# Kernel tuning notes

Hardware: AMD Instinct MI355X
Metric: run time of the kernel (lower is better)

Reference implementation:

```python
import jax, jax.numpy as jnp
import numpy as np

D, M, K, L, H, BS = 128, 8, 256, 2, 256, 1024


def setup_inputs() -> dict:
    key = jax.random.key(0)
    ks = jax.random.split(key, 7)
    s_d = 1.0 / np.sqrt(D)
    s_2d = 1.0 / np.sqrt(2 * D)
    s_h = 1.0 / np.sqrt(H)
    x = jax.random.normal(ks[0], (BS, D), jnp.float32)
    codebook0 = jax.random.uniform(ks[1], (K, D), jnp.float32, -s_d, s_d)
    codebooks = jax.random.uniform(ks[2], (M - 1, K, D), jnp.float32, -s_d, s_d)
    Wc = jax.random.uniform(ks[3], (M - 1, D, 2 * D), jnp.float32, -s_2d, s_2d)
    bc = jax.random.uniform(ks[4], (M - 1, D), jnp.float32, -s_2d, s_2d)
    W1 = jax.random.uniform(ks[5], (M - 1, L, H, D), jnp.float32, -s_d, s_d)
    W2 = jax.random.uniform(ks[6], (M - 1, L, D, H), jnp.float32, -s_h, s_h)
    return {"x": x, "codebook0": codebook0, "codebooks": codebooks,
            "Wc": Wc, "bc": bc, "W1": W1, "W2": W2}


def _step_targets(xhat, cb, Wc_m, bc_m, W1_m, W2_m):
    """Candidate quantization targets for one step. xhat:[bs,d], cb:[K,d] -> [bs,K,d].
    MLPconcat(concat(zqs, xhat)) is split into the zqs part and the xhat part so the
    [bs*K, 2d] repeat of the torch code is never materialized (same math)."""
    Wz, Wx = Wc_m[:, :D], Wc_m[:, D:]          # Linear(2d,d): y = cc @ W.T + b
    z = cb[None, :, :] + (cb @ Wz.T)[None, :, :] + (xhat @ Wx.T)[:, None, :] + bc_m  # [bs,K,d]
    for l in range(L):
        z = z + jnp.maximum(jnp.einsum('bkd,hd->bkh', z, W1_m[l]), 0.0) @ W2_m[l].T
    return z + xhat[:, None, :]


def _encode(x, codebook0, codebooks, Wc, bc, W1, W2):
    # step 0: plain nearest-centroid assignment (assign_to_codebook)
    d0 = (x * x).sum(-1, keepdims=True) + (codebook0 * codebook0).sum(-1) - 2.0 * x @ codebook0.T
    code0 = jnp.argmin(d0, axis=1)
    xhat = codebook0[code0]
    codes = [code0]
    xn = (x * x).sum(-1, keepdims=True)        # [bs,1]
    for m in range(M - 1):
        z = _step_targets(xhat, codebooks[m], Wc[m], bc[m], W1[m], W2[m])  # [bs,K,d]
        dist = xn + (z * z).sum(-1) - 2.0 * jnp.einsum('bd,bkd->bk', x, z)
        idx = jnp.argmin(dist, axis=1)
        xhat = jnp.take_along_axis(z, idx[:, None, None], axis=1)[:, 0, :]
        codes.append(idx)
    return jnp.stack(codes, axis=1)            # [bs, M] int


def _decode(codes, codebook0, codebooks, Wc, bc, W1, W2):
    xhat = codebook0[codes[:, 0]]
    side = [xhat]
    for m in range(M - 1):
        zq = codebooks[m][codes[:, m + 1]]     # [bs,d]
        Wz, Wx = Wc[m][:, :D], Wc[m][:, D:]
        z = zq + zq @ Wz.T + xhat @ Wx.T + bc[m]
        for l in range(L):
            z = z + jnp.maximum(z @ W1[m, l].T, 0.0) @ W2[m, l].T
        xhat = xhat + z
        side.append(xhat)
    return xhat, side


def reference(x, codebook0, codebooks, Wc, bc, W1, W2):
    # forward(): encode under no_grad, then differentiable decode with side outputs
    codes = jax.lax.stop_gradient(_encode(x, codebook0, codebooks, Wc, bc, W1, W2))
    xhat, side = _decode(codes, codebook0, codebooks, Wc, bc, W1, W2)
    return (xhat, codes, tuple(side))
```

## Files before the change

### kernel.cpp

```cpp
#include <hip/hip_runtime.h>


typedef _Float16 f16;
typedef f16 half4_t __attribute__((ext_vector_type(4)));
typedef f16 half8_t __attribute__((ext_vector_type(8)));
typedef float f32x16 __attribute__((ext_vector_type(16)));

#define OUT_CODES 131072
#define OUT_SIDE  139264

#define WS_XHAT  0
#define WS_RB    131072
#define WS_Y     262144
#define WS_ZC    393216
#define WS_BESTD 425984
#define WS_BESTI 430080
#define WS_BESTZ 434176
#define WS_WSPLIT 960000
#define NW1 458752

#define HLO 8192

__device__ __forceinline__ f32x16 mfma_f16(half8_t a, half8_t b, f32x16 c) {
  return __builtin_amdgcn_mfma_f32_32x32x16_f16(a, b, c, 0, 0, 0);
}

__global__ __launch_bounds__(256) void k_wsplit(const float* __restrict__ W1,
    const float* __restrict__ W2, f16* __restrict__ wsh)
{
  int i = (blockIdx.x * 256 + threadIdx.x) * 4;
  const float* src;
  f16* hi;
  if (i < NW1) { src = W1 + i; hi = wsh + i; }
  else         { src = W2 + (i - NW1); hi = wsh + 2 * NW1 + (i - NW1); }
  f16* lo = hi + NW1;
  float4 v = *(const float4*)src;
  half4_t h, l;
  float s;
  s = v.x * 256.f; h[0] = (f16)s; l[0] = (f16)(s - (float)h[0]);
  s = v.y * 256.f; h[1] = (f16)s; l[1] = (f16)(s - (float)h[1]);
  s = v.z * 256.f; h[2] = (f16)s; l[2] = (f16)(s - (float)h[2]);
  s = v.w * 256.f; h[3] = (f16)s; l[3] = (f16)(s - (float)h[3]);
  *(half4_t*)hi = h;
  *(half4_t*)lo = l;
}

__global__ __launch_bounds__(256) void k_step0(const float* __restrict__ x,
    const float* __restrict__ cb0, float* __restrict__ ws, float* __restrict__ out)
{
  __shared__ float xs[128];
  __shared__ float redv[4];
  __shared__ int   redi[4];
  __shared__ int   kwin;
  int tx = threadIdx.x, b = blockIdx.x;
  if (tx < 128) xs[tx] = x[b * 128 + tx];
  __syncthreads();
  const float* c = cb0 + tx * 128;
  float s = 0.f;
  for (int d = 0; d < 128; d += 4) {
    float4 cv = *(const float4*)(c + d);
    float4 xv = *(const float4*)(xs + d);
    float a0 = xv.x - cv.x, a1 = xv.y - cv.y, a2 = xv.z - cv.z, a3 = xv.w - cv.w;
    s += a0 * a0 + a1 * a1 + a2 * a2 + a3 * a3;
  }
  float v = s; int idx = tx;
  for (int off = 32; off; off >>= 1) {
    float v2 = __shfl_xor(v, off);
    int   i2 = __shfl_xor(idx, off);
    if (v2 < v || (v2 == v && i2 < idx)) { v = v2; idx = i2; }
  }
  if ((tx & 63) == 0) { redv[tx >> 6] = v; redi[tx >> 6] = idx; }
  __syncthreads();
  if (tx == 0) {
    float bv = redv[0]; int bi = redi[0];
    for (int w = 1; w < 4; w++)
      if (redv[w] < bv || (redv[w] == bv && redi[w] < bi)) { bv = redv[w]; bi = redi[w]; }
    kwin = bi;
    out[OUT_CODES + b * 8] = (float)bi;
  }
  __syncthreads();
  int k = kwin;
  if (tx < 128) {
    float xh = cb0[k * 128 + tx];
    ws[WS_XHAT + b * 128 + tx] = xh;
    ws[WS_RB   + b * 128 + tx] = xs[tx] - xh;
    out[OUT_SIDE + b * 128 + tx] = xh;
  }
}

__global__ __launch_bounds__(128) void k_prep(const float* __restrict__ cb,
    const float* __restrict__ Wc, const float* __restrict__ bcm, float* __restrict__ ws)
{
  __shared__ float row[128];
  int tx = threadIdx.x, blk = blockIdx.x;
  if (blk < 256) {
    row[tx] = cb[blk * 128 + tx];
    __syncthreads();
    const float* wrow = Wc + tx * 256;
    float s = 0.f;
    for (int d = 0; d < 128; d += 4) {
      float4 wv = *(const float4*)(wrow + d);
      float4 zv = *(const float4*)(row + d);
      s += wv.x * zv.x + wv.y * zv.y + wv.z * zv.z + wv.w * zv.w;
    }
    ws[WS_ZC + blk * 128 + tx] = row[tx] + s + bcm[tx];
  } else {
    int b = blk - 256;
    row[tx] = ws[WS_XHAT + b * 128 + tx];
    __syncthreads();
    const float* wrow = Wc + tx * 256 + 128;
    float s = 0.f;
    for (int d = 0; d < 128; d += 4) {
      float4 wv = *(const float4*)(wrow + d);
      float4 zv = *(const float4*)(row + d);
      s += wv.x * zv.x + wv.y * zv.y + wv.z * zv.z + wv.w * zv.w;
    }
    ws[WS_Y + b * 128 + tx] = s;
  }
}

__global__ __launch_bounds__(256, 2) void k_step(const f16* __restrict__ wsh,
    float* __restrict__ ws, int sm)
{
  __shared__ __align__(16) f16 lds[32768];
  f16* Zh = lds;
  f16* Zl = lds + HLO;
  f16* Hh = lds + 2 * HLO;
  f16* Hl = lds + 3 * HLO;
  int tx = threadIdx.x;
  int lane = tx & 63, w = tx >> 6;
  int col = lane & 31, koct = lane >> 5;
  int b = blockIdx.x >> 2, t = blockIdx.x & 3, k0 = t << 6;

  {
    const float* zc = ws + WS_ZC + k0 * 128;
    const float* y  = ws + WS_Y + b * 128;
    for (int idx = tx; idx < 1024; idx += 256) {
      int m = idx & 63, d0 = (idx >> 6) << 3;
      float4 a  = *(const float4*)(zc + m * 128 + d0);
      float4 bb = *(const float4*)(zc + m * 128 + d0 + 4);
      float4 ya = *(const float4*)(y + d0);
      float4 yb = *(const float4*)(y + d0 + 4);
      float sv[8] = {a.x + ya.x, a.y + ya.y, a.z + ya.z, a.w + ya.w,
                     bb.x + yb.x, bb.y + yb.y, bb.z + yb.z, bb.w + yb.w};
      half8_t h8, l8;
#pragma unroll
      for (int j = 0; j < 8; j++) {
        float v = sv[j] * 256.f;
        f16 h = (f16)v; h8[j] = h; l8[j] = (f16)(v - (float)h);
      }
      int c0 = (d0 + ((m & 15) << 3)) & 127;
      *(half8_t*)(Zh + (m << 7) + c0) = h8;
      *(half8_t*)(Zl + (m << 7) + c0) = l8;
    }
  }
  __syncthreads();

  const int rot0 = (col & 15) << 3;
  const f16* Zr0 = Zh + (col << 7);
  const f16* Zr1 = Zh + ((col + 32) << 7);
  const f16* Hr0 = Hh + (col << 7);
  const f16* Hr1 = Hh + ((col + 32) << 7);

  for (int l = 0; l < 2; l++) {
    const f16* w1h = wsh + (size_t)((sm * 2 + l) * 256) * 128;
    const f16* w2h = wsh + 2 * NW1 + (size_t)((sm * 2 + l) * 128) * 256;
    f32x16 acc2[2];
#pragma unroll
    for (int i = 0; i < 16; i++) { acc2[0][i] = 0.f; acc2[1][i] = 0.f; }

#pragma unroll
    for (int hf = 0; hf < 2; hf++) {
      const f16* a1p = w1h + (size_t)((hf << 7) + (w << 5) + col) * 128 + (koct << 3);
      const f16* a2p = w2h + (size_t)((w << 5) + col) * 256 + (hf << 7) + (koct << 3);
      half8_t a1hv[8], a1lv[8], a2hv[8], a2lv[8];
#pragma unroll
      for (int kc = 0; kc < 8; kc++) {
        a1hv[kc] = *(const half8_t*)(a1p + (kc << 4));
        a1lv[kc] = *(const half8_t*)(a1p + NW1 + (kc << 4));
      }
#pragma unroll
      for (int kc = 0; kc < 8; kc++) {
        a2hv[kc] = *(const half8_t*)(a2p + (kc << 4));
        a2lv[kc] = *(const half8_t*)(a2p + NW1 + (kc << 4));
      }

      f32x16 acc1[2];
#pragma unroll
      for (int i = 0; i < 16; i++) { acc1[0][i] = 0.f; acc1[1][i] = 0.f; }
#pragma unroll
      for (int kc = 0; kc < 8; kc++) {
        int poff = (((kc << 4) + (koct << 3)) + rot0) & 127;
        half8_t bh0 = *(const half8_t*)(Zr0 + poff);
        half8_t bl0 = *(const half8_t*)(Zr0 + HLO + poff);
        half8_t bh1 = *(const half8_t*)(Zr1 + poff);
        half8_t bl1 = *(const half8_t*)(Zr1 + HLO + poff);
        acc1[0] = mfma_f16(a1hv[kc], bh0, acc1[0]);
        acc1[1] = mfma_f16(a1hv[kc], bh1, acc1[1]);
        acc1[0] = mfma_f16(a1lv[kc], bh0, acc1[0]);
        acc1[1] = mfma_f16(a1lv[kc], bh1, acc1[1]);
        acc1[0] = mfma_f16(a1hv[kc], bl0, acc1[0]);
        acc1[1] = mfma_f16(a1hv[kc], bl1, acc1[1]);
      }
#pragma unroll
      for (int mt = 0; mt < 2; mt++) {
        int m = (mt << 5) + col;
#pragma unroll
        for (int qd = 0; qd < 4; qd++) {
          half4_t hv, lv;
#pragma unroll
          for (int j = 0; j < 4; j++) {
            float tv = fmaxf(acc1[mt][(qd << 2) + j], 0.f) * 0.00390625f;
            f16 h = (f16)tv; hv[j] = h; lv[j] = (f16)(tv - (float)h);
          }
          int c = (((w << 5) + (qd << 3) + (koct << 2)) + rot0) & 127;
          *(half4_t*)(Hh + (m << 7) + c) = hv;
          *(half4_t*)(Hl + (m << 7) + c) = lv;
        }
      }
      __syncthreads();
#pragma unroll
      for (int kc = 0; kc < 8; kc++) {
        int poff = (((kc << 4) + (koct << 3)) + rot0) & 127;
        half8_t bh0 = *(const half8_t*)(Hr0 + poff);
        half8_t bl0 = *(const half8_t*)(Hr0 + HLO + poff);
        half8_t bh1 = *(const half8_t*)(Hr1 + poff);
        half8_t bl1 = *(const half8_t*)(Hr1 + HLO + poff);
        acc2[0] = mfma_f16(a2hv[kc], bh0, acc2[0]);
        acc2[1] = mfma_f16(a2hv[kc], bh1, acc2[1]);
        acc2[0] = mfma_f16(a2lv[kc], bh0, acc2[0]);
        acc2[1] = mfma_f16(a2lv[kc], bh1, acc2[1]);
        acc2[0] = mfma_f16(a2hv[kc], bl0, acc2[0]);
        acc2[1] = mfma_f16(a2hv[kc], bl1, acc2[1]);
      }
      __syncthreads();
    }
#pragma unroll
    for (int mt = 0; mt < 2; mt++) {
      int m = (mt << 5) + col;
      f16* zhr = Zh + (m << 7);
      f16* zlr = Zl + (m << 7);
#pragma unroll
      for (int qd = 0; qd < 4; qd++) {
        int c = (((w << 5) + (qd << 3) + (koct << 2)) + rot0) & 127;
        half4_t zh = *(half4_t*)(zhr + c);
        half4_t zl = *(half4_t*)(zlr + c);
#pragma unroll
        for (int j = 0; j < 4; j++) {
          float zs = (float)zh[j] + (float)zl[j];
          zs += acc2[mt][(qd << 2) + j] * 0.00390625f;
          f16 h = (f16)zs; zh[j] = h; zl[j] = (f16)(zs - (float)h);
        }
        *(half4_t*)(zhr + c) = zh;
        *(half4_t*)(zlr + c) = zl;
      }
    }
    __syncthreads();
  }

  float* pd = (float*)Hh;
  int* rwin = (int*)Hh + 64;
  {
    int row = tx >> 2, seg = tx & 3;
    int rotr = (row & 15) << 3;
    const f16* zhr = Zh + (row << 7);
    const f16* zlr = Zl + (row << 7);
    const float* rb = ws + WS_RB + b * 128 + (seg << 5);
    float s = 0.f;
#pragma unroll
    for (int o = 0; o < 4; o++) {
      int c = (((seg << 5) + (o << 3)) + rotr) & 127;
      half8_t zh = *(const half8_t*)(zhr + c);
      half8_t zl = *(const half8_t*)(zlr + c);
      float4 r0 = *(const float4*)(rb + (o << 3));
      float4 r1 = *(const float4*)(rb + (o << 3) + 4);
      float rr[8] = {r0.x, r0.y, r0.z, r0.w, r1.x, r1.y, r1.z, r1.w};
#pragma unroll
      for (int j = 0; j < 8; j++) {
        float z = ((float)zh[j] + (float)zl[j]) * 0.00390625f;
        float dlt = rr[j] - z;
        s += dlt * dlt;
      }
    }
    s += __shfl_xor(s, 1);
    s += __shfl_xor(s, 2);
    if (seg == 0) pd[row] = s;
  }
  __syncthreads();
  if (tx < 64) {
    float v = pd[tx]; int idx = tx;
#pragma unroll
    for (int off = 32; off; off >>= 1) {
      float v2 = __shfl_xor(v, off);
      int   i2 = __shfl_xor(idx, off);
      if (v2 < v || (v2 == v && i2 < idx)) { v = v2; idx = i2; }
    }
    if (tx == 0) {
      ws[WS_BESTD + (b << 2) + t] = v;
      ((int*)ws)[WS_BESTI + (b << 2) + t] = k0 + idx;
      rwin[0] = idx;
    }
  }
  __syncthreads();
  if (tx < 32) {
    int rw = rwin[0];
    int c = ((tx << 2) + ((rw & 15) << 3)) & 127;
    half4_t zh = *(const half4_t*)(Zh + (rw << 7) + c);
    half4_t zl = *(const half4_t*)(Zl + (rw << 7) + c);
    float4 z;
    z.x = ((float)zh[0] + (float)zl[0]) * 0.00390625f;
    z.y = ((float)zh[1] + (float)zl[1]) * 0.00390625f;
    z.z = ((float)zh[2] + (float)zl[2]) * 0.00390625f;
    z.w = ((float)zh[3] + (float)zl[3]) * 0.00390625f;
    *(float4*)(ws + WS_BESTZ + (((b << 2) + t) << 7) + (tx << 2)) = z;
  }
}

__global__ __launch_bounds__(128) void k_update(const float* __restrict__ x,
    float* __restrict__ ws, float* __restrict__ out, int m, int last)
{
  __shared__ int tsel;
  int tx = threadIdx.x, b = blockIdx.x;
  if (tx == 0) {
    float bv = ws[WS_BESTD + (b << 2)]; int bt = 0;
    for (int q = 1; q < 4; q++) {
      float v = ws[WS_BESTD + (b << 2) + q];
      if (v < bv) { bv = v; bt = q; }
    }
    tsel = bt;
    int k = ((const int*)ws)[WS_BESTI + (b << 2) + bt];
    out[OUT_CODES + b * 8 + (m + 1)] = (float)k;
  }
  __syncthreads();
  int bt = tsel;
  float z  = ws[WS_BESTZ + (((b << 2) + bt) << 7) + tx];
  float xh = ws[WS_XHAT + b * 128 + tx] + z;
  ws[WS_XHAT + b * 128 + tx] = xh;
  ws[WS_RB   + b * 128 + tx] = x[b * 128 + tx] - xh;
  out[OUT_SIDE + (m + 1) * 131072 + b * 128 + tx] = xh;
  if (last) out[b * 128 + tx] = xh;
}

extern "C" void kernel_launch(void* const* d_in, const int* in_sizes, int n_in,
                              void* d_out, int out_size, void* d_ws, size_t ws_size,
                              hipStream_t stream)
{
  const float* x   = (const float*)d_in[0];
  const float* cb0 = (const float*)d_in[1];
  const float* cbs = (const float*)d_in[2];
  const float* Wc  = (const float*)d_in[3];
  const float* bc  = (const float*)d_in[4];
  const float* W1  = (const float*)d_in[5];
  const float* W2  = (const float*)d_in[6];
  float* out = (float*)d_out;
  float* ws  = (float*)d_ws;
  f16* wsh = (f16*)(ws + WS_WSPLIT);

  k_wsplit<<<896, 256, 0, stream>>>(W1, W2, wsh);
  k_step0<<<1024, 256, 0, stream>>>(x, cb0, ws, out);
  for (int m = 0; m < 7; m++) {
    k_prep<<<1280, 128, 0, stream>>>(cbs + m * 256 * 128, Wc + m * 128 * 256,
                                     bc + m * 128, ws);
    k_step<<<4096, 256, 0, stream>>>(wsh, ws, m);
    k_update<<<1024, 128, 0, stream>>>(x, ws, out, m, (m == 6) ? 1 : 0);
  }
}
```

Before: 2.151 ms.

## Software-pipeline MLP hidden halves and raise wave priority around MFMA loops

```diff
diff --git a/kernel.cpp b/kernel.cpp
--- a/kernel.cpp
+++ b/kernel.cpp
@@ -169,72 +169,147 @@
 #pragma unroll
     for (int i = 0; i < 16; i++) { acc2[0][i] = 0.f; acc2[1][i] = 0.f; }
 
-#pragma unroll
-    for (int hf = 0; hf < 2; hf++) {
-      const f16* a1p = w1h + (size_t)((hf << 7) + (w << 5) + col) * 128 + (koct << 3);
-      const f16* a2p = w2h + (size_t)((w << 5) + col) * 256 + (hf << 7) + (koct << 3);
-      half8_t a1hv[8], a1lv[8], a2hv[8], a2lv[8];
+    half8_t a1hv[8], a1lv[8];
+    {
+      const f16* a1p = w1h + (size_t)((w << 5) + col) * 128 + (koct << 3);
 #pragma unroll
       for (int kc = 0; kc < 8; kc++) {
         a1hv[kc] = *(const half8_t*)(a1p + (kc << 4));
         a1lv[kc] = *(const half8_t*)(a1p + NW1 + (kc << 4));
       }
+    }
+
+    f32x16 acc1[2];
+#pragma unroll
+    for (int i = 0; i < 16; i++) { acc1[0][i] = 0.f; acc1[1][i] = 0.f; }
+    __builtin_amdgcn_s_setprio(1);
+#pragma unroll
+    for (int kc = 0; kc < 8; kc++) {
+      int poff = (((kc << 4) + (koct << 3)) + rot0) & 127;
+      half8_t bh0 = *(const half8_t*)(Zr0 + poff);
+      half8_t bl0 = *(const half8_t*)(Zr0 + HLO + poff);
+      half8_t bh1 = *(const half8_t*)(Zr1 + poff);
+      half8_t bl1 = *(const half8_t*)(Zr1 + HLO + poff);
+      acc1[0] = mfma_f16(a1hv[kc], bh0, acc1[0]);
+      acc1[1] = mfma_f16(a1hv[kc], bh1, acc1[1]);
+      acc1[0] = mfma_f16(a1lv[kc], bh0, acc1[0]);
+      acc1[1] = mfma_f16(a1lv[kc], bh1, acc1[1]);
+      acc1[0] = mfma_f16(a1hv[kc], bl0, acc1[0]);
+      acc1[1] = mfma_f16(a1hv[kc], bl1, acc1[1]);
+    }
+    __builtin_amdgcn_s_setprio(0);
+
+    half8_t a2hv[8], a2lv[8];
+    {
+      const f16* a2p = w2h + (size_t)((w << 5) + col) * 256 + (koct << 3);
 #pragma unroll
       for (int kc = 0; kc < 8; kc++) {
         a2hv[kc] = *(const half8_t*)(a2p + (kc << 4));
         a2lv[kc] = *(const half8_t*)(a2p + NW1 + (kc << 4));
       }
-
-      f32x16 acc1[2];
-#pragma unroll
-      for (int i = 0; i < 16; i++) { acc1[0][i] = 0.f; acc1[1][i] = 0.f; }
+    }
+    half8_t b1hv[8], b1lv[8];
+    {
+      const f16* b1p = w1h + (size_t)(128 + (w << 5) + col) * 128 + (koct << 3);
 #pragma unroll
       for (int kc = 0; kc < 8; kc++) {
-        int poff = (((kc << 4) + (koct << 3)) + rot0) & 127;
-        half8_t bh0 = *(const half8_t*)(Zr0 + poff);
-        half8_t bl0 = *(const half8_t*)(Zr0 + HLO + poff);
-        half8_t bh1 = *(const half8_t*)(Zr1 + poff);
-        half8_t bl1 = *(const half8_t*)(Zr1 + HLO + poff);
-        acc1[0] = mfma_f16(a1hv[kc], bh0, acc1[0]);
-        acc1[1] = mfma_f16(a1hv[kc], bh1, acc1[1]);
-        acc1[0] = mfma_f16(a1lv[kc], bh0, acc1[0]);
-        acc1[1] = mfma_f16(a1lv[kc], bh1, acc1[1]);
-        acc1[0] = mfma_f16(a1hv[kc], bl0, acc1[0]);
-        acc1[1] = mfma_f16(a1hv[kc], bl1, acc1[1]);
-      }
-#pragma unroll
-      for (int mt = 0; mt < 2; mt++) {
-        int m = (mt << 5) + col;
-#pragma unroll
-        for (int qd = 0; qd < 4; qd++) {
-          half4_t hv, lv;
-#pragma unroll
-          for (int j = 0; j < 4; j++) {
-            float tv = fmaxf(acc1[mt][(qd << 2) + j], 0.f) * 0.00390625f;
-            f16 h = (f16)tv; hv[j] = h; lv[j] = (f16)(tv - (float)h);
-          }
-          int c = (((w << 5) + (qd << 3) + (koct << 2)) + rot0) & 127;
-          *(half4_t*)(Hh + (m << 7) + c) = hv;
-          *(half4_t*)(Hl + (m << 7) + c) = lv;
+        b1hv[kc] = *(const half8_t*)(b1p + (kc << 4));
+        b1lv[kc] = *(const half8_t*)(b1p + NW1 + (kc << 4));
+      }
+    }
+
+#pragma unroll
+    for (int mt = 0; mt < 2; mt++) {
+      int m = (mt << 5) + col;
+#pragma unroll
+      for (int qd = 0; qd < 4; qd++) {
+        half4_t hv, lv;
+#pragma unroll
+        for (int j = 0; j < 4; j++) {
+          float tv = fmaxf(acc1[mt][(qd << 2) + j], 0.f) * 0.00390625f;
+          f16 h = (f16)tv; hv[j] = h; lv[j] = (f16)(tv - (float)h);
         }
-      }
-      __syncthreads();
+        int c = (((w << 5) + (qd << 3) + (koct << 2)) + rot0) & 127;
+        *(half4_t*)(Hh + (m << 7) + c) = hv;
+        *(half4_t*)(Hl + (m << 7) + c) = lv;
+      }
+    }
+    __syncthreads();
+
+#pragma unroll
+    for (int i = 0; i < 16; i++) { acc1[0][i] = 0.f; acc1[1][i] = 0.f; }
+    __builtin_amdgcn_s_setprio(1);
+#pragma unroll
+    for (int kc = 0; kc < 8; kc++) {
+      int poff = (((kc << 4) + (koct << 3)) + rot0) & 127;
+      half8_t hh0 = *(const half8_t*)(Hr0 + poff);
+      half8_t hl0 = *(const half8_t*)(Hr0 + HLO + poff);
+      half8_t hh1 = *(const half8_t*)(Hr1 + poff);
+      half8_t hl1 = *(const half8_t*)(Hr1 + HLO + poff);
+      half8_t zh0 = *(const half8_t*)(Zr0 + poff);
+      half8_t zl0 = *(const half8_t*)(Zr0 + HLO + poff);
+      half8_t zh1 = *(const half8_t*)(Zr1 + poff);
+      half8_t zl1 = *(const half8_t*)(Zr1 + HLO + poff);
+      acc2[0] = mfma_f16(a2hv[kc], hh0, acc2[0]);
+      acc1[0] = mfma_f16(b1hv[kc], zh0, acc1[0]);
+      acc2[1] = mfma_f16(a2hv[kc], hh1, acc2[1]);
+      acc1[1] = mfma_f16(b1hv[kc], zh1, acc1[1]);
+      acc2[0] = mfma_f16(a2lv[kc], hh0, acc2[0]);
+      acc1[0] = mfma_f16(b1lv[kc], zh0, acc1[0]);
+      acc2[1] = mfma_f16(a2lv[kc], hh1, acc2[1]);
+      acc1[1] = mfma_f16(b1lv[kc], zh1, acc1[1]);
+      acc2[0] = mfma_f16(a2hv[kc], hl0, acc2[0]);
+      acc1[0] = mfma_f16(b1hv[kc], zl0, acc1[0]);
+      acc2[1] = mfma_f16(a2hv[kc], hl1, acc2[1]);
+      acc1[1] = mfma_f16(b1hv[kc], zl1, acc1[1]);
+    }
+    __builtin_amdgcn_s_setprio(0);
+
+    {
+      const f16* a2q = w2h + (size_t)((w << 5) + col) * 256 + 128 + (koct << 3);
 #pragma unroll
       for (int kc = 0; kc < 8; kc++) {
-        int poff = (((kc << 4) + (koct << 3)) + rot0) & 127;
-        half8_t bh0 = *(const half8_t*)(Hr0 + poff);
-        half8_t bl0 = *(const half8_t*)(Hr0 + HLO + poff);
-        half8_t bh1 = *(const half8_t*)(Hr1 + poff);
-        half8_t bl1 = *(const half8_t*)(Hr1 + HLO + poff);
-        acc2[0] = mfma_f16(a2hv[kc], bh0, acc2[0]);
-        acc2[1] = mfma_f16(a2hv[kc], bh1, acc2[1]);
-        acc2[0] = mfma_f16(a2lv[kc], bh0, acc2[0]);
-        acc2[1] = mfma_f16(a2lv[kc], bh1, acc2[1]);
-        acc2[0] = mfma_f16(a2hv[kc], bl0, acc2[0]);
-        acc2[1] = mfma_f16(a2hv[kc], bl1, acc2[1]);
-      }
-      __syncthreads();
-    }
+        a2hv[kc] = *(const half8_t*)(a2q + (kc << 4));
+        a2lv[kc] = *(const half8_t*)(a2q + NW1 + (kc << 4));
+      }
+    }
+    __syncthreads();
+
+#pragma unroll
+    for (int mt = 0; mt < 2; mt++) {
+      int m = (mt << 5) + col;
+#pragma unroll
+      for (int qd = 0; qd < 4; qd++) {
+        half4_t hv, lv;
+#pragma unroll
+        for (int j = 0; j < 4; j++) {
+          float tv = fmaxf(acc1[mt][(qd << 2) + j], 0.f) * 0.00390625f;
+          f16 h = (f16)tv; hv[j] = h; lv[j] = (f16)(tv - (float)h);
+        }
+        int c = (((w << 5) + (qd << 3) + (koct << 2)) + rot0) & 127;
+        *(half4_t*)(Hh + (m << 7) + c) = hv;
+        *(half4_t*)(Hl + (m << 7) + c) = lv;
+      }
+    }
+    __syncthreads();
+
+    __builtin_amdgcn_s_setprio(1);
+#pragma unroll
+    for (int kc = 0; kc < 8; kc++) {
+      int poff = (((kc << 4) + (koct << 3)) + rot0) & 127;
+      half8_t bh0 = *(const half8_t*)(Hr0 + poff);
+      half8_t bl0 = *(const half8_t*)(Hr0 + HLO + poff);
+      half8_t bh1 = *(const half8_t*)(Hr1 + poff);
+      half8_t bl1 = *(const half8_t*)(Hr1 + HLO + poff);
+      acc2[0] = mfma_f16(a2hv[kc], bh0, acc2[0]);
+      acc2[1] = mfma_f16(a2hv[kc], bh1, acc2[1]);
+      acc2[0] = mfma_f16(a2lv[kc], bh0, acc2[0]);
+      acc2[1] = mfma_f16(a2lv[kc], bh1, acc2[1]);
+      acc2[0] = mfma_f16(a2hv[kc], bl0, acc2[0]);
+      acc2[1] = mfma_f16(a2hv[kc], bl1, acc2[1]);
+    }
+    __builtin_amdgcn_s_setprio(0);
+
 #pragma unroll
     for (int mt = 0; mt < 2; mt++) {
       int m = (mt << 5) + col;
```

Result: slower. 2.449 ms (+13.8%).

## Split hidden dimension into four quarters to shrink LDS and raise occupancy

Applied to the files above, without the earlier changes.

```diff
diff --git a/kernel.cpp b/kernel.cpp
--- a/kernel.cpp
+++ b/kernel.cpp
@@ -19,7 +19,8 @@
 #define WS_WSPLIT 960000
 #define NW1 458752
 
-#define HLO 8192
+#define ZLO 8192
+#define HLOQ 4096
 
 __device__ __forceinline__ f32x16 mfma_f16(half8_t a, half8_t b, f32x16 c) {
   return __builtin_amdgcn_mfma_f32_32x32x16_f16(a, b, c, 0, 0, 0);
@@ -119,14 +120,14 @@
   }
 }
 
-__global__ __launch_bounds__(256, 2) void k_step(const f16* __restrict__ wsh,
+__global__ __launch_bounds__(256, 3) void k_step(const f16* __restrict__ wsh,
     float* __restrict__ ws, int sm)
 {
-  __shared__ __align__(16) f16 lds[32768];
+  __shared__ __align__(16) f16 lds[24576];
   f16* Zh = lds;
-  f16* Zl = lds + HLO;
-  f16* Hh = lds + 2 * HLO;
-  f16* Hl = lds + 3 * HLO;
+  f16* Zl = lds + ZLO;
+  f16* Hh = lds + 2 * ZLO;
+  f16* Hl = Hh + HLOQ;
   int tx = threadIdx.x;
   int lane = tx & 63, w = tx >> 6;
   int col = lane & 31, koct = lane >> 5;
@@ -157,10 +158,15 @@
   __syncthreads();
 
   const int rot0 = (col & 15) << 3;
-  const f16* Zr0 = Zh + (col << 7);
-  const f16* Zr1 = Zh + ((col + 32) << 7);
-  const f16* Hr0 = Hh + (col << 7);
-  const f16* Hr1 = Hh + ((col + 32) << 7);
+  const int rotH = (col & 7) << 3;
+  const int mrow1 = ((w & 1) << 5) + col;
+  const f16* Zg1 = Zh + (mrow1 << 7);
+  const int rotG1 = (col & 15) << 3;
+  const f16* Hr0 = Hh + (col << 6);
+  const f16* Hr1 = Hh + ((col + 32) << 6);
+
+  float* pd = (float*)Hh;
+  int* rwin = (int*)Hh + 64;
 
   for (int l = 0; l < 2; l++) {
     const f16* w1h = wsh + (size_t)((sm * 2 + l) * 256) * 128;
@@ -169,63 +175,78 @@
 #pragma unroll
     for (int i = 0; i < 16; i++) { acc2[0][i] = 0.f; acc2[1][i] = 0.f; }
 
-#pragma unroll
-    for (int hf = 0; hf < 2; hf++) {
-      const f16* a1p = w1h + (size_t)((hf << 7) + (w << 5) + col) * 128 + (koct << 3);
-      const f16* a2p = w2h + (size_t)((w << 5) + col) * 256 + (hf << 7) + (koct << 3);
-      half8_t a1hv[8], a1lv[8], a2hv[8], a2lv[8];
+    half8_t a1hv[8], a1lv[8];
+    {
+      const f16* a1p = w1h + (size_t)(((w >> 1) << 5) + col) * 128 + (koct << 3);
 #pragma unroll
       for (int kc = 0; kc < 8; kc++) {
         a1hv[kc] = *(const half8_t*)(a1p + (kc << 4));
         a1lv[kc] = *(const half8_t*)(a1p + NW1 + (kc << 4));
       }
+    }
+
+#pragma unroll
+    for (int q = 0; q < 4; q++) {
+      f32x16 acc1;
+#pragma unroll
+      for (int i = 0; i < 16; i++) acc1[i] = 0.f;
+      __builtin_amdgcn_s_setprio(1);
 #pragma unroll
       for (int kc = 0; kc < 8; kc++) {
-        a2hv[kc] = *(const half8_t*)(a2p + (kc << 4));
-        a2lv[kc] = *(const half8_t*)(a2p + NW1 + (kc << 4));
-      }
-
-      f32x16 acc1[2];
-#pragma unroll
-      for (int i = 0; i < 16; i++) { acc1[0][i] = 0.f; acc1[1][i] = 0.f; }
-#pragma unroll
-      for (int kc = 0; kc < 8; kc++) {
-        int poff = (((kc << 4) + (koct << 3)) + rot0) & 127;
-        half8_t bh0 = *(const half8_t*)(Zr0 + poff);
-        half8_t bl0 = *(const half8_t*)(Zr0 + HLO + poff);
-        half8_t bh1 = *(const half8_t*)(Zr1 + poff);
-        half8_t bl1 = *(const half8_t*)(Zr1 + HLO + poff);
-        acc1[0] = mfma_f16(a1hv[kc], bh0, acc1[0]);
-        acc1[1] = mfma_f16(a1hv[kc], bh1, acc1[1]);
-        acc1[0] = mfma_f16(a1lv[kc], bh0, acc1[0]);
-        acc1[1] = mfma_f16(a1lv[kc], bh1, acc1[1]);
-        acc1[0] = mfma_f16(a1hv[kc], bl0, acc1[0]);
-        acc1[1] = mfma_f16(a1hv[kc], bl1, acc1[1]);
-      }
-#pragma unroll
-      for (int mt = 0; mt < 2; mt++) {
-        int m = (mt << 5) + col;
+        int poff = (((kc << 4) + (koct << 3)) + rotG1) & 127;
+        half8_t bh = *(const half8_t*)(Zg1 + poff);
+        half8_t bl = *(const half8_t*)(Zg1 + ZLO + poff);
+        acc1 = mfma_f16(a1hv[kc], bh, acc1);
+        acc1 = mfma_f16(a1lv[kc], bh, acc1);
+        acc1 = mfma_f16(a1hv[kc], bl, acc1);
+      }
+      __builtin_amdgcn_s_setprio(0);
+
+      half8_t a2hv[4], a2lv[4];
+      {
+        const f16* a2p = w2h + (size_t)((w << 5) + col) * 256 + (q << 6) + (koct << 3);
+#pragma unroll
+        for (int kc = 0; kc < 4; kc++) {
+          a2hv[kc] = *(const half8_t*)(a2p + (kc << 4));
+          a2lv[kc] = *(const half8_t*)(a2p + NW1 + (kc << 4));
+        }
+      }
+      if (q < 3) {
+        const f16* a1p = w1h + (size_t)(((q + 1) << 6) + ((w >> 1) << 5) + col) * 128
+                       + (koct << 3);
+#pragma unroll
+        for (int kc = 0; kc < 8; kc++) {
+          a1hv[kc] = *(const half8_t*)(a1p + (kc << 4));
+          a1lv[kc] = *(const half8_t*)(a1p + NW1 + (kc << 4));
+        }
+      }
+
+      {
+        int m = ((w & 1) << 5) + col;
 #pragma unroll
         for (int qd = 0; qd < 4; qd++) {
           half4_t hv, lv;
 #pragma unroll
           for (int j = 0; j < 4; j++) {
-            float tv = fmaxf(acc1[mt][(qd << 2) + j], 0.f) * 0.00390625f;
+            float tv = fmaxf(acc1[(qd << 2) + j], 0.f) * 0.00390625f;
             f16 h = (f16)tv; hv[j] = h; lv[j] = (f16)(tv - (float)h);
           }
-          int c = (((w << 5) + (qd << 3) + (koct << 2)) + rot0) & 127;
-          *(half4_t*)(Hh + (m << 7) + c) = hv;
-          *(half4_t*)(Hl + (m << 7) + c) = lv;
+          int hb = ((w >> 1) << 5) + (qd << 3) + (koct << 2);
+          int c = (hb + rotH) & 63;
+          *(half4_t*)(Hh + (m << 6) + c) = hv;
+          *(half4_t*)(Hl + (m << 6) + c) = lv;
         }
       }
       __syncthreads();
-#pragma unroll
-      for (int kc = 0; kc < 8; kc++) {
-        int poff = (((kc << 4) + (koct << 3)) + rot0) & 127;
+
+      __builtin_amdgcn_s_setprio(1);
+#pragma unroll
+      for (int kc = 0; kc < 4; kc++) {
+        int poff = (((kc << 4) + (koct << 3)) + rotH) & 63;
         half8_t bh0 = *(const half8_t*)(Hr0 + poff);
-        half8_t bl0 = *(const half8_t*)(Hr0 + HLO + poff);
+        half8_t bl0 = *(const half8_t*)(Hr0 + HLOQ + poff);
         half8_t bh1 = *(const half8_t*)(Hr1 + poff);
-        half8_t bl1 = *(const half8_t*)(Hr1 + HLO + poff);
+        half8_t bl1 = *(const half8_t*)(Hr1 + HLOQ + poff);
         acc2[0] = mfma_f16(a2hv[kc], bh0, acc2[0]);
         acc2[1] = mfma_f16(a2hv[kc], bh1, acc2[1]);
         acc2[0] = mfma_f16(a2lv[kc], bh0, acc2[0]);
@@ -233,8 +254,10 @@
         acc2[0] = mfma_f16(a2hv[kc], bl0, acc2[0]);
         acc2[1] = mfma_f16(a2hv[kc], bl1, acc2[1]);
       }
-      __syncthreads();
-    }
+      __builtin_amdgcn_s_setprio(0);
+      if (q < 3) __syncthreads();
+    }
+
 #pragma unroll
     for (int mt = 0; mt < 2; mt++) {
       int m = (mt << 5) + col;
@@ -258,8 +281,6 @@
     __syncthreads();
   }
 
-  float* pd = (float*)Hh;
-  int* rwin = (int*)Hh + 64;
   {
     int row = tx >> 2, seg = tx & 3;
     int rotr = (row & 15) << 3;
```

Measured after the change: 3.091 ms. 43.7% more time.
